# Performance work log

Hardware: AMD Instinct MI355X
Metric: run time of the kernel (lower is better)

Reference implementation:

```python
import jax, jax.numpy as jnp
import numpy as np

B, L, D, H = 16, 1024, 1024, 16
HD = D // H  # head dim = 64


def setup_inputs() -> dict:
    rng = jax.random.key(0)
    ks = jax.random.split(rng, 12)
    s = 0.02
    return {
        "key": jax.random.normal(ks[0], (B, L, D), jnp.float32),
        "value": jax.random.normal(ks[1], (B, L, D), jnp.float32),
        "query": jax.random.normal(ks[2], (B, L, D), jnp.float32),
        "atten_masks": jax.random.randint(ks[3], (B, L, L), 0, 2, jnp.int32),
        "Wk": jax.random.normal(ks[4], (D, D), jnp.float32) * s,
        "bk": jnp.zeros((D,), jnp.float32),
        "Wq": jax.random.normal(ks[5], (D, D), jnp.float32) * s,
        "bq": jnp.zeros((D,), jnp.float32),
        "Wv": jax.random.normal(ks[6], (D, D), jnp.float32) * s,
        "bv": jnp.zeros((D,), jnp.float32),
        "Wp": jax.random.normal(ks[7], (D, D), jnp.float32) * s,
        "bp": jnp.zeros((D,), jnp.float32),
    }


def reference(key, value, query, atten_masks, Wk, bk, Wq, bq, Wv, bv, Wp, bp):
    # Linear projections (torch nn.Linear: x @ W^T + b)
    def lin(x, W, b):
        return x @ W.T + b

    # [B, L, D] -> [B, H, L, HD]
    def heads(x):
        return x.reshape(B, L, H, HD).transpose(0, 2, 1, 3)

    k = heads(lin(key, Wk, bk))
    q = heads(lin(query, Wq, bq))
    v = heads(lin(value, Wv, bv))

    scale = 1.0 / np.sqrt(HD).astype(np.float32)
    att = jnp.einsum("bhqd,bhkd->bhqk", q, k) * scale  # [B, H, L, L]
    att = jnp.where(atten_masks[:, None, :, :] == 0, -jnp.inf, att)
    att = jax.nn.softmax(att, axis=-1)

    y = jnp.einsum("bhqk,bhkd->bhqd", att, v)  # [B, H, L, HD]
    y = y.transpose(0, 2, 1, 3).reshape(B, L, D)
    return lin(y, Wp, bp)
```

## Files before the change

kernel.cpp:

```cpp
#include <hip/hip_runtime.h>

typedef __bf16 bf16_t;
typedef __bf16 bf16x4 __attribute__((ext_vector_type(4)));
typedef __bf16 bf16x8 __attribute__((ext_vector_type(8)));
typedef float f32x4 __attribute__((ext_vector_type(4)));
typedef float f32x16 __attribute__((ext_vector_type(16)));
typedef unsigned u32x2 __attribute__((ext_vector_type(2)));

#define QSCALE 0.18033688f

__device__ __forceinline__ int swz(int row) { return (row ^ (row >> 3)) & 7; }
__device__ __forceinline__ int swz2(int row) { return (row ^ (row >> 2)) & 3; }
__device__ __forceinline__ int swzv(int row) { return (row ^ (row >> 3)) & 15; }

__device__ __forceinline__ f32x4 mfma16(bf16x8 a, bf16x8 b, f32x4 c) {
  return __builtin_amdgcn_mfma_f32_16x16x32_bf16(a, b, c, 0, 0, 0);
}
__device__ __forceinline__ f32x16 mfma32(bf16x8 a, bf16x8 b, f32x16 c) {
  return __builtin_amdgcn_mfma_f32_32x32x16_bf16(a, b, c, 0, 0, 0);
}

__device__ __forceinline__ void gl_lds16(const void* g, void* l) {
  __builtin_amdgcn_global_load_lds(
      (const __attribute__((address_space(1))) unsigned int*)g,
      (__attribute__((address_space(3))) unsigned int*)l, 16, 0, 0);
}

__global__ __launch_bounds__(256) void cvt_all_kernel(
    const float* __restrict__ key, const float* __restrict__ query,
    const float* __restrict__ value, const float* __restrict__ Wk,
    const float* __restrict__ Wq, const float* __restrict__ Wv,
    const float* __restrict__ Wp, const int* __restrict__ mask,
    bf16_t* __restrict__ I1, bf16_t* __restrict__ I2, bf16_t* __restrict__ I3,
    bf16_t* __restrict__ Wkb, bf16_t* __restrict__ Wqb,
    bf16_t* __restrict__ Wvb, bf16_t* __restrict__ Wpb,
    unsigned* __restrict__ mbits) {
  const int bid = blockIdx.x;
  if (bid >= 53248) {
    int idx = (bid - 53248) * 256 + threadIdx.x;
    const int4* src = (const int4*)(mask + (size_t)idx * 32);
    unsigned w = 0;
#pragma unroll
    for (int i = 0; i < 8; ++i) {
      int4 v = src[i];
      w |= (v.x != 0 ? 1u : 0u) << (i * 4 + 0);
      w |= (v.y != 0 ? 1u : 0u) << (i * 4 + 1);
      w |= (v.z != 0 ? 1u : 0u) << (i * 4 + 2);
      w |= (v.w != 0 ? 1u : 0u) << (i * 4 + 3);
    }
    mbits[idx] = w;
    return;
  }
  const float* s;
  bf16_t* d;
  int base;
  float sc = 1.0f;
  if (bid < 16384) { s = key; d = I1; base = bid; }
  else if (bid < 32768) { s = query; d = I2; base = bid - 16384; }
  else if (bid < 49152) { s = value; d = I3; base = bid - 32768; }
  else if (bid < 50176) { s = Wk; d = Wkb; base = bid - 49152; }
  else if (bid < 51200) { s = Wq; d = Wqb; base = bid - 50176; sc = QSCALE; }
  else if (bid < 52224) { s = Wv; d = Wvb; base = bid - 51200; }
  else { s = Wp; d = Wpb; base = bid - 52224; }
  int i = base * 256 + threadIdx.x;
  float4 v = ((const float4*)s)[i];
  bf16x4 o;
  o[0] = (bf16_t)(v.x * sc); o[1] = (bf16_t)(v.y * sc);
  o[2] = (bf16_t)(v.z * sc); o[3] = (bf16_t)(v.w * sc);
  ((bf16x4*)d)[i] = o;
}

template <typename OT>
__device__ __forceinline__ void gemm256_body(const bf16_t* __restrict__ A,
                                             const bf16_t* __restrict__ W,
                                             const float* __restrict__ bias,
                                             float bscale,
                                             OT* __restrict__ O) {
  extern __shared__ __align__(16) char smem[];
  bf16_t* AsBase = (bf16_t*)smem;
  bf16_t* BsBase = (bf16_t*)(smem + 3 * 8192 * 2);

  const int t = threadIdx.x;
  const int lane = t & 63;
  const int wid = t >> 6;
  const int g = lane >> 4;
  const int lr = lane & 15;
  const int wm = wid >> 2, wn = wid & 3;
  const int lid = blockIdx.x;
  const int logical = (lid & 7) * 64 + (lid >> 3);
  const int m0 = (logical >> 3) * 256;
  const int n0 = (logical & 7) * 128;

  f32x4 acc[8][2] = {};

  auto STAGE = [&](int buf, int kb) {
    bf16_t* Ab = AsBase + buf * 8192;
    bf16_t* Bb = BsBase + buf * 4096;
#pragma unroll
    for (int rr = 0; rr < 2; ++rr) {
      int s = rr * 512 + t;
      int row = s >> 2, c = s & 3;
      gl_lds16(A + (size_t)(m0 + row) * 1024 + kb + (c ^ swz2(row)) * 8,
               &Ab[(rr * 512 + wid * 64) * 8]);
    }
    {
      int row = t >> 2, c = t & 3;
      gl_lds16(W + (size_t)(n0 + row) * 1024 + kb + (c ^ swz2(row)) * 8,
               &Bb[(wid * 64 + lane) * 8]);
    }
  };

  STAGE(0, 0);
  STAGE(1, 32);

  int cur = 0;
  for (int kb = 0; kb < 1024; kb += 32) {
    if (kb + 32 < 1024)
      asm volatile("s_waitcnt vmcnt(3)" ::: "memory");
    else
      asm volatile("s_waitcnt vmcnt(0)" ::: "memory");
    __builtin_amdgcn_sched_barrier(0);
    __builtin_amdgcn_s_barrier();
    __builtin_amdgcn_sched_barrier(0);

    if (kb + 64 < 1024) {
      int fut = cur + 2;
      if (fut >= 3) fut -= 3;
      STAGE(fut, kb + 64);
    }

    const bf16_t* Ab = AsBase + cur * 8192;
    const bf16_t* Bb = BsBase + cur * 4096;
    bf16x8 a[8], b[2];
#pragma unroll
    for (int i = 0; i < 8; ++i) {
      int row = wm * 128 + i * 16 + lr;
      a[i] = *(const bf16x8*)&Ab[row * 32 + ((g ^ swz2(row))) * 8];
    }
#pragma unroll
    for (int j = 0; j < 2; ++j) {
      int row = wn * 32 + j * 16 + lr;
      b[j] = *(const bf16x8*)&Bb[row * 32 + ((g ^ swz2(row))) * 8];
    }
    __builtin_amdgcn_s_setprio(1);
#pragma unroll
    for (int i = 0; i < 8; ++i)
#pragma unroll
      for (int j = 0; j < 2; ++j)
        acc[i][j] = mfma16(a[i], b[j], acc[i][j]);
    __builtin_amdgcn_s_setprio(0);

    cur = cur + 1;
    if (cur >= 3) cur -= 3;
  }

  float bval[2];
#pragma unroll
  for (int j = 0; j < 2; ++j)
    bval[j] = bias[n0 + wn * 32 + j * 16 + lr] * bscale;
#pragma unroll
  for (int i = 0; i < 8; ++i)
#pragma unroll
    for (int r = 0; r < 4; ++r) {
      int row = m0 + wm * 128 + i * 16 + g * 4 + r;
#pragma unroll
      for (int j = 0; j < 2; ++j) {
        int n = n0 + wn * 32 + j * 16 + lr;
        O[(size_t)row * 1024 + n] = (OT)(acc[i][j][r] + bval[j]);
      }
    }
}

__global__ __launch_bounds__(512, 2) void gemm256_qkv_kernel(
    const bf16_t* key, const bf16_t* query, const bf16_t* value,
    const bf16_t* Wkb, const bf16_t* Wqb, const bf16_t* Wvb, const float* bk,
    const float* bq, const float* bv, bf16_t* ko, bf16_t* qo, bf16_t* vo) {
  const bf16_t *A, *W;
  const float* bi;
  bf16_t* O;
  float bs = 1.0f;
  if (blockIdx.y == 0) { A = key; W = Wkb; bi = bk; O = ko; }
  else if (blockIdx.y == 1) { A = query; W = Wqb; bi = bq; O = qo; bs = QSCALE; }
  else { A = value; W = Wvb; bi = bv; O = vo; }
  gemm256_body<bf16_t>(A, W, bi, bs, O);
}

__global__ __launch_bounds__(512, 2) void gemm256_out_kernel(
    const bf16_t* __restrict__ A, const bf16_t* __restrict__ W,
    const float* __restrict__ b, float* __restrict__ O) {
  gemm256_body<float>(A, W, b, 1.0f, O);
}

__global__ __launch_bounds__(256) void transpose_v_kernel(
    const bf16_t* __restrict__ v_ws, bf16_t* __restrict__ vT) {
  __shared__ bf16_t T[64 * 66];
  const int kc = blockIdx.x, h = blockIdx.y, b = blockIdx.z;
  const int t = threadIdx.x;
  {
    int key = t >> 2, dblk = t & 3;
    const bf16_t* src =
        v_ws + ((size_t)(b * 1024 + kc * 64 + key)) * 1024 + h * 64 + dblk * 16;
    bf16x8 a0 = *(const bf16x8*)src;
    bf16x8 a1 = *(const bf16x8*)(src + 8);
    bf16_t* row = &T[key * 66 + dblk * 16];
#pragma unroll
    for (int j = 0; j < 4; ++j) {
      ((unsigned*)row)[j] = ((const unsigned*)&a0)[j];
      ((unsigned*)row)[j + 4] = ((const unsigned*)&a1)[j];
    }
  }
  __syncthreads();
  {
    int d = t >> 2, kcl = t & 3;
    bf16x8 o0, o1;
#pragma unroll
    for (int e = 0; e < 8; ++e) {
      o0[e] = T[(kcl * 16 + e) * 66 + d];
      o1[e] = T[(kcl * 16 + 8 + e) * 66 + d];
    }
    bf16_t* dst =
        vT + ((size_t)((b * 16 + h) * 64 + d)) * 1024 + kc * 64 + kcl * 16;
    *(bf16x8*)dst = o0;
    *(bf16x8*)(dst + 8) = o1;
  }
}

__global__ __launch_bounds__(512) void attn_kernel(
    const bf16_t* __restrict__ q_ws, const bf16_t* __restrict__ k_ws,
    const bf16_t* __restrict__ vT, const unsigned* __restrict__ mbits,
    bf16_t* __restrict__ y_ws) {
  __shared__ __align__(16) bf16_t Ks[128 * 64];
  __shared__ __align__(16) bf16_t Vs[64 * 128];

  const int lid = blockIdx.x;
  const int logical = (lid & 7) * 128 + (lid >> 3);
  const int qb = logical & 3;
  const int h = (logical >> 2) & 15;
  const int b = logical >> 6;
  const int t = threadIdx.x, lane = t & 63, wid = t >> 6;
  const int ql = lane & 31;
  const int hh = lane >> 5;
  const int q = qb * 256 + wid * 32 + ql;

  bf16x8 qf[4];
  {
    const bf16_t* qp = q_ws + ((size_t)(b * 1024 + q)) * 1024 + h * 64 + hh * 8;
#pragma unroll
    for (int kc = 0; kc < 4; ++kc) qf[kc] = *(const bf16x8*)(qp + kc * 16);
  }

  bf16x8 onesf;
#pragma unroll
  for (int e = 0; e < 8; ++e) onesf[e] = (bf16_t)1.0f;

  f32x16 acc0 = {}, acc1 = {}, accl = {};
  const bf16_t* Kb = k_ws + ((size_t)b * 1024) * 1024 + h * 64;
  const bf16_t* Vb = vT + ((size_t)((b * 16 + h) * 64)) * 1024;
  const unsigned* mrow = mbits + ((size_t)(b * 1024 + q)) * 32;

  for (int kb = 0; kb < 8; ++kb) {
    __syncthreads();
#pragma unroll
    for (int rr = 0; rr < 2; ++rr) {
      int s = rr * 512 + t;
      int row = s >> 3, c = s & 7;
      gl_lds16(Kb + (size_t)(kb * 128 + row) * 1024 + (c ^ swz(row)) * 8,
               &Ks[(rr * 512 + wid * 64) * 8]);
    }
#pragma unroll
    for (int rr = 0; rr < 2; ++rr) {
      int s = rr * 512 + t;
      int row = s >> 4, c = s & 15;
      gl_lds16(Vb + (size_t)row * 1024 + kb * 128 + ((c ^ swzv(row))) * 8,
               &Vs[(rr * 512 + wid * 64) * 8]);
    }
    uint4 mw = *(const uint4*)&mrow[kb * 4];
    __syncthreads();

#pragma unroll
    for (int ct = 0; ct < 4; ++ct) {
      f32x16 c = {};
      __builtin_amdgcn_s_setprio(1);
#pragma unroll
      for (int kc = 0; kc < 4; ++kc) {
        int row = ct * 32 + ql;
        bf16x8 kf = *(const bf16x8*)&Ks[row * 64 + (((kc * 2 + hh) ^ swz(row))) * 8];
        c = mfma32(kf, qf[kc], c);
      }
      __builtin_amdgcn_s_setprio(0);

      unsigned w = ((const unsigned*)&mw)[ct] >> (4 * hh);
      float p[16];
#pragma unroll
      for (int r = 0; r < 16; ++r) {
        const int posr = (r & 3) + 8 * (r >> 2);
        int nm = (int)(w << (31 - posr)) >> 31;
        float e0 = __builtin_amdgcn_exp2f(c[r]);
        p[r] = __int_as_float(__float_as_int(e0) & nm);
      }

      bf16x8 pbt[2];
#pragma unroll
      for (int j = 0; j < 2; ++j) {
        const int base = j * 8;
        union { bf16_t h[2]; unsigned u; } a0, a1, b0, b1;
        a0.h[0] = (bf16_t)p[base + 0]; a0.h[1] = (bf16_t)p[base + 1];
        a1.h[0] = (bf16_t)p[base + 2]; a1.h[1] = (bf16_t)p[base + 3];
        b0.h[0] = (bf16_t)p[base + 4]; b0.h[1] = (bf16_t)p[base + 5];
        b1.h[0] = (bf16_t)p[base + 6]; b1.h[1] = (bf16_t)p[base + 7];
        u32x2 s0 = __builtin_amdgcn_permlane32_swap(a0.u, b0.u, false, false);
        u32x2 s1 = __builtin_amdgcn_permlane32_swap(a1.u, b1.u, false, false);
        union { unsigned u[4]; bf16x8 v; } pk;
        pk.u[0] = s0.x;
        pk.u[1] = s1.x;
        pk.u[2] = s0.y;
        pk.u[3] = s1.y;
        pbt[j] = pk.v;
      }

      __builtin_amdgcn_s_setprio(1);
#pragma unroll
      for (int j = 0; j < 2; ++j) {
        int sl = (2 * ct + j) * 2 + hh;
        {
          int row = ql;
          bf16x8 vf = *(const bf16x8*)&Vs[row * 128 + ((sl ^ swzv(row))) * 8];
          acc0 = mfma32(vf, pbt[j], acc0);
        }
        {
          int row = 32 + ql;
          bf16x8 vf = *(const bf16x8*)&Vs[row * 128 + ((sl ^ swzv(row))) * 8];
          acc1 = mfma32(vf, pbt[j], acc1);
        }
        accl = mfma32(onesf, pbt[j], accl);
      }
      __builtin_amdgcn_s_setprio(0);
    }
  }

  float inv = 1.0f / fmaxf(accl[0], 1e-30f);
  bf16_t* yp = y_ws + ((size_t)(b * 1024 + q)) * 1024 + h * 64;
#pragma unroll
  for (int j = 0; j < 4; ++j) {
    bf16x4 o0, o1;
#pragma unroll
    for (int e = 0; e < 4; ++e) {
      o0[e] = (bf16_t)(acc0[4 * j + e] * inv);
      o1[e] = (bf16_t)(acc1[4 * j + e] * inv);
    }
    *(bf16x4*)&yp[8 * j + 4 * hh] = o0;
    *(bf16x4*)&yp[32 + 8 * j + 4 * hh] = o1;
  }
}

extern "C" void kernel_launch(void* const* d_in, const int* in_sizes, int n_in,
                              void* d_out, int out_size, void* d_ws,
                              size_t ws_size, hipStream_t stream) {
  (void)in_sizes; (void)n_in; (void)out_size; (void)ws_size;
  const float* key = (const float*)d_in[0];
  const float* value = (const float*)d_in[1];
  const float* query = (const float*)d_in[2];
  const int* mask = (const int*)d_in[3];
  const float* Wk = (const float*)d_in[4];
  const float* bk = (const float*)d_in[5];
  const float* Wq = (const float*)d_in[6];
  const float* bq = (const float*)d_in[7];
  const float* Wv = (const float*)d_in[8];
  const float* bv = (const float*)d_in[9];
  const float* Wp = (const float*)d_in[10];
  const float* bp = (const float*)d_in[11];
  float* out = (float*)d_out;

  char* ws = (char*)d_ws;
  const size_t MB = 1ull << 20;
  unsigned* mbits = (unsigned*)(ws);
  bf16_t* Wkb = (bf16_t*)(ws + 2 * MB);
  bf16_t* Wqb = (bf16_t*)(ws + 4 * MB);
  bf16_t* Wvb = (bf16_t*)(ws + 6 * MB);
  bf16_t* Wpb = (bf16_t*)(ws + 8 * MB);
  bf16_t* I1 = (bf16_t*)(ws + 10 * MB);
  bf16_t* I2 = (bf16_t*)(ws + 42 * MB);
  bf16_t* I3 = (bf16_t*)(ws + 74 * MB);
  bf16_t* k_ws = (bf16_t*)(ws + 106 * MB);
  bf16_t* q_ws = (bf16_t*)(ws + 138 * MB);
  bf16_t* v_ws = (bf16_t*)(ws + 170 * MB);
  bf16_t* vT_ws = I1;
  bf16_t* y_ws = I2;

  const size_t GEMM_LDS = 3 * (8192 + 4096) * 2;

  cvt_all_kernel<<<55296, 256, 0, stream>>>(key, query, value, Wk, Wq, Wv, Wp,
                                            mask, I1, I2, I3, Wkb, Wqb, Wvb,
                                            Wpb, mbits);
  gemm256_qkv_kernel<<<dim3(512, 3), 512, GEMM_LDS, stream>>>(
      I1, I2, I3, Wkb, Wqb, Wvb, bk, bq, bv, k_ws, q_ws, v_ws);
  transpose_v_kernel<<<dim3(16, 16, 16), 256, 0, stream>>>(v_ws, vT_ws);
  attn_kernel<<<1024, 512, 0, stream>>>(q_ws, k_ws, vT_ws, mbits, y_ws);
  gemm256_out_kernel<<<512, 512, GEMM_LDS, stream>>>(y_ws, Wpb, bp, out);
}
```

Before: 348.3 us.

## Fuse V transpose into QKV GEMM epilogue and coarsen conversion kernel

The V projection GEMM now writes its output directly in transposed [b,h,d,l] layout from the epilogue using bf16x4 stores, which removes the separate transpose kernel and its extra read and write of V. The fp32-to-bf16 conversion kernel now has each block handle four float4 chunks per thread instead of one, cutting the block count by four. The transposed stores write 8 bytes per lane at a stride of one output row, so they may coalesce worse than the row-major stores used for K and Q.

```diff
diff --git a/kernel.cpp b/kernel.cpp
--- a/kernel.cpp
+++ b/kernel.cpp
@@ -36,8 +36,8 @@
     bf16_t* __restrict__ Wvb, bf16_t* __restrict__ Wpb,
     unsigned* __restrict__ mbits) {
   const int bid = blockIdx.x;
-  if (bid >= 53248) {
-    int idx = (bid - 53248) * 256 + threadIdx.x;
+  if (bid >= 13312) {
+    int idx = (bid - 13312) * 256 + threadIdx.x;
     const int4* src = (const int4*)(mask + (size_t)idx * 32);
     unsigned w = 0;
 #pragma unroll
@@ -55,22 +55,25 @@
   bf16_t* d;
   int base;
   float sc = 1.0f;
-  if (bid < 16384) { s = key; d = I1; base = bid; }
-  else if (bid < 32768) { s = query; d = I2; base = bid - 16384; }
-  else if (bid < 49152) { s = value; d = I3; base = bid - 32768; }
-  else if (bid < 50176) { s = Wk; d = Wkb; base = bid - 49152; }
-  else if (bid < 51200) { s = Wq; d = Wqb; base = bid - 50176; sc = QSCALE; }
-  else if (bid < 52224) { s = Wv; d = Wvb; base = bid - 51200; }
-  else { s = Wp; d = Wpb; base = bid - 52224; }
-  int i = base * 256 + threadIdx.x;
-  float4 v = ((const float4*)s)[i];
-  bf16x4 o;
-  o[0] = (bf16_t)(v.x * sc); o[1] = (bf16_t)(v.y * sc);
-  o[2] = (bf16_t)(v.z * sc); o[3] = (bf16_t)(v.w * sc);
-  ((bf16x4*)d)[i] = o;
-}
-
-template <typename OT>
+  if (bid < 4096) { s = key; d = I1; base = bid; }
+  else if (bid < 8192) { s = query; d = I2; base = bid - 4096; }
+  else if (bid < 12288) { s = value; d = I3; base = bid - 8192; }
+  else if (bid < 12544) { s = Wk; d = Wkb; base = bid - 12288; }
+  else if (bid < 12800) { s = Wq; d = Wqb; base = bid - 12544; sc = QSCALE; }
+  else if (bid < 13056) { s = Wv; d = Wvb; base = bid - 12800; }
+  else { s = Wp; d = Wpb; base = bid - 13056; }
+#pragma unroll
+  for (int k = 0; k < 4; ++k) {
+    int i = base * 1024 + k * 256 + threadIdx.x;
+    float4 v = ((const float4*)s)[i];
+    bf16x4 o;
+    o[0] = (bf16_t)(v.x * sc); o[1] = (bf16_t)(v.y * sc);
+    o[2] = (bf16_t)(v.z * sc); o[3] = (bf16_t)(v.w * sc);
+    ((bf16x4*)d)[i] = o;
+  }
+}
+
+template <typename OT, bool VT>
 __device__ __forceinline__ void gemm256_body(const bf16_t* __restrict__ A,
                                              const bf16_t* __restrict__ W,
                                              const float* __restrict__ bias,
@@ -158,71 +161,52 @@
 #pragma unroll
   for (int j = 0; j < 2; ++j)
     bval[j] = bias[n0 + wn * 32 + j * 16 + lr] * bscale;
-#pragma unroll
-  for (int i = 0; i < 8; ++i)
-#pragma unroll
-    for (int r = 0; r < 4; ++r) {
-      int row = m0 + wm * 128 + i * 16 + g * 4 + r;
+
+  if constexpr (VT) {
+    const int bb = m0 >> 10;
+    const int lbase = (m0 & 1023) + wm * 128;
+#pragma unroll
+    for (int i = 0; i < 8; ++i)
 #pragma unroll
       for (int j = 0; j < 2; ++j) {
         int n = n0 + wn * 32 + j * 16 + lr;
-        O[(size_t)row * 1024 + n] = (OT)(acc[i][j][r] + bval[j]);
-      }
-    }
+        bf16x4 o;
+#pragma unroll
+        for (int r = 0; r < 4; ++r) o[r] = (bf16_t)(acc[i][j][r] + bval[j]);
+        *(bf16x4*)&O[((size_t)(bb * 1024 + n)) * 1024 + lbase + i * 16 + g * 4] = o;
+      }
+  } else {
+#pragma unroll
+    for (int i = 0; i < 8; ++i)
+#pragma unroll
+      for (int r = 0; r < 4; ++r) {
+        int row = m0 + wm * 128 + i * 16 + g * 4 + r;
+#pragma unroll
+        for (int j = 0; j < 2; ++j) {
+          int n = n0 + wn * 32 + j * 16 + lr;
+          O[(size_t)row * 1024 + n] = (OT)(acc[i][j][r] + bval[j]);
+        }
+      }
+  }
 }
 
 __global__ __launch_bounds__(512, 2) void gemm256_qkv_kernel(
     const bf16_t* key, const bf16_t* query, const bf16_t* value,
     const bf16_t* Wkb, const bf16_t* Wqb, const bf16_t* Wvb, const float* bk,
-    const float* bq, const float* bv, bf16_t* ko, bf16_t* qo, bf16_t* vo) {
-  const bf16_t *A, *W;
-  const float* bi;
-  bf16_t* O;
-  float bs = 1.0f;
-  if (blockIdx.y == 0) { A = key; W = Wkb; bi = bk; O = ko; }
-  else if (blockIdx.y == 1) { A = query; W = Wqb; bi = bq; O = qo; bs = QSCALE; }
-  else { A = value; W = Wvb; bi = bv; O = vo; }
-  gemm256_body<bf16_t>(A, W, bi, bs, O);
+    const float* bq, const float* bv, bf16_t* ko, bf16_t* qo, bf16_t* vTo) {
+  if (blockIdx.y == 0) {
+    gemm256_body<bf16_t, false>(key, Wkb, bk, 1.0f, ko);
+  } else if (blockIdx.y == 1) {
+    gemm256_body<bf16_t, false>(query, Wqb, bq, QSCALE, qo);
+  } else {
+    gemm256_body<bf16_t, true>(value, Wvb, bv, 1.0f, vTo);
+  }
 }
 
 __global__ __launch_bounds__(512, 2) void gemm256_out_kernel(
     const bf16_t* __restrict__ A, const bf16_t* __restrict__ W,
     const float* __restrict__ b, float* __restrict__ O) {
-  gemm256_body<float>(A, W, b, 1.0f, O);
-}
-
-__global__ __launch_bounds__(256) void transpose_v_kernel(
-    const bf16_t* __restrict__ v_ws, bf16_t* __restrict__ vT) {
-  __shared__ bf16_t T[64 * 66];
-  const int kc = blockIdx.x, h = blockIdx.y, b = blockIdx.z;
-  const int t = threadIdx.x;
-  {
-    int key = t >> 2, dblk = t & 3;
-    const bf16_t* src =
-        v_ws + ((size_t)(b * 1024 + kc * 64 + key)) * 1024 + h * 64 + dblk * 16;
-    bf16x8 a0 = *(const bf16x8*)src;
-    bf16x8 a1 = *(const bf16x8*)(src + 8);
-    bf16_t* row = &T[key * 66 + dblk * 16];
-#pragma unroll
-    for (int j = 0; j < 4; ++j) {
-      ((unsigned*)row)[j] = ((const unsigned*)&a0)[j];
-      ((unsigned*)row)[j + 4] = ((const unsigned*)&a1)[j];
-    }
-  }
-  __syncthreads();
-  {
-    int d = t >> 2, kcl = t & 3;
-    bf16x8 o0, o1;
-#pragma unroll
-    for (int e = 0; e < 8; ++e) {
-      o0[e] = T[(kcl * 16 + e) * 66 + d];
-      o1[e] = T[(kcl * 16 + 8 + e) * 66 + d];
-    }
-    bf16_t* dst =
-        vT + ((size_t)((b * 16 + h) * 64 + d)) * 1024 + kc * 64 + kcl * 16;
-    *(bf16x8*)dst = o0;
-    *(bf16x8*)(dst + 8) = o1;
-  }
+  gemm256_body<float, false>(A, W, b, 1.0f, O);
 }
 
 __global__ __launch_bounds__(512) void attn_kernel(
@@ -383,18 +367,16 @@
   bf16_t* I3 = (bf16_t*)(ws + 74 * MB);
   bf16_t* k_ws = (bf16_t*)(ws + 106 * MB);
   bf16_t* q_ws = (bf16_t*)(ws + 138 * MB);
-  bf16_t* v_ws = (bf16_t*)(ws + 170 * MB);
-  bf16_t* vT_ws = I1;
+  bf16_t* vT_ws = (bf16_t*)(ws + 170 * MB);
   bf16_t* y_ws = I2;
 
   const size_t GEMM_LDS = 3 * (8192 + 4096) * 2;
 
-  cvt_all_kernel<<<55296, 256, 0, stream>>>(key, query, value, Wk, Wq, Wv, Wp,
+  cvt_all_kernel<<<15360, 256, 0, stream>>>(key, query, value, Wk, Wq, Wv, Wp,
                                             mask, I1, I2, I3, Wkb, Wqb, Wvb,
                                             Wpb, mbits);
   gemm256_qkv_kernel<<<dim3(512, 3), 512, GEMM_LDS, stream>>>(
-      I1, I2, I3, Wkb, Wqb, Wvb, bk, bq, bv, k_ws, q_ws, v_ws);
-  transpose_v_kernel<<<dim3(16, 16, 16), 256, 0, stream>>>(v_ws, vT_ws);
+      I1, I2, I3, Wkb, Wqb, Wvb, bk, bq, bv, k_ws, q_ws, vT_ws);
   attn_kernel<<<1024, 512, 0, stream>>>(q_ws, k_ws, vT_ws, mbits, y_ws);
   gemm256_out_kernel<<<512, 512, GEMM_LDS, stream>>>(y_ws, Wpb, bp, out);
 }
```

After: 363.9 us. 4.5% more time.
